# Performance work log

Measured on AMD Instinct MI355X. Metric: run time of the kernel, lower is better.

## Reference

```python
import jax, jax.numpy as jnp
import numpy as np

N, E = 25000, 400000
NF, EF, HNF, HEF = 32, 32, 128, 128
NOUT, EOUT = 32, 32
D_N, D_E = HNF + NF, HEF + EF  # concat dims fed to the GNN layer


def _glorot(key, shape):
    return jax.random.normal(key, shape, jnp.float32) / np.sqrt(shape[0])


def setup_inputs() -> dict:
    key = jax.random.key(0)
    ks = jax.random.split(key, 10)
    return {
        "nf": jax.random.normal(ks[0], (N, NF), jnp.float32),
        "ef": jax.random.normal(ks[1], (E, EF), jnp.float32),
        "src": jax.random.randint(ks[2], (E,), 0, N),
        "dst": jax.random.randint(ks[3], (E,), 0, N),
        # AttnMPNNLayer params: edge model, attention logit model, node model
        "W_edge": _glorot(ks[4], (2 * D_N + D_E, HEF)),
        "b_edge": jnp.zeros((HEF,), jnp.float32),
        "W_attn": _glorot(ks[5], (2 * D_N + D_E, 1)),
        "b_attn": jnp.zeros((1,), jnp.float32),
        "W_node": _glorot(ks[6], (D_N + HEF, HNF)),
        "b_node": jnp.zeros((HNF,), jnp.float32),
        # output heads (MLP with num_neurons=[] -> single Linear)
        "W_nout": _glorot(ks[7], (HNF, NOUT)),
        "b_nout": jnp.zeros((NOUT,), jnp.float32),
        "W_eout": _glorot(ks[8], (HEF, EOUT)),
        "b_eout": jnp.zeros((EOUT,), jnp.float32),
        "n_iters": 3,
    }


def _attn_mpnn_layer(hnf, hef, src, dst, W_edge, b_edge, W_attn, b_attn, W_node, b_node):
    """Attention message passing: gather endpoints, edge MLP + attn logit,
    edge-softmax over incoming edges (per dst node), scatter-aggregate, node MLP."""
    n = hnf.shape[0]
    e_in = jnp.concatenate([hnf[src], hnf[dst], hef], axis=-1)   # [E, 2*D_N + D_E]
    m = jax.nn.relu(e_in @ W_edge + b_edge)                      # [E, HEF] new edge feats
    logit = (e_in @ W_attn + b_attn)[:, 0]                       # [E]
    # numerically stable edge softmax grouped by destination node
    lmax = jax.ops.segment_max(logit, dst, num_segments=n)
    lmax = jnp.where(jnp.isfinite(lmax), lmax, 0.0)              # isolated nodes -> 0
    a = jnp.exp(logit - lmax[dst])
    denom = jax.ops.segment_sum(a, dst, num_segments=n)
    alpha = a / jnp.maximum(denom[dst], 1e-16)
    agg = jax.ops.segment_sum(alpha[:, None] * m, dst, num_segments=n)  # [N, HEF]
    un = jax.nn.relu(jnp.concatenate([hnf, agg], axis=-1) @ W_node + b_node)  # [N, HNF]
    return un, m


def reference(nf, ef, src, dst, W_edge, b_edge, W_attn, b_attn, W_node, b_node,
              W_nout, b_nout, W_eout, b_eout, n_iters):
    hnf = jnp.zeros((nf.shape[0], HNF), nf.dtype)
    hef = jnp.zeros((ef.shape[0], HEF), ef.dtype)
    for _ in range(n_iters):
        hnf = jnp.concatenate([hnf, nf], axis=-1)   # input re-injection
        hef = jnp.concatenate([hef, ef], axis=-1)
        hnf, hef = _attn_mpnn_layer(hnf, hef, src, dst,
                                    W_edge, b_edge, W_attn, b_attn, W_node, b_node)
    unf = hnf @ W_nout + b_nout
    uef = hef @ W_eout + b_eout
    return unf, uef
```

## Files before the change

kernel.cpp:

```cpp
#include <hip/hip_runtime.h>


#define GN 25000
#define GE 400000
#define NODE_BLKS 196
#define EDGE_BLKS 6250

typedef unsigned short u16;
typedef __attribute__((ext_vector_type(8))) short bf16x8;
typedef __attribute__((ext_vector_type(4))) float f32x4;

__device__ inline float b2f(u16 v) {
  union { unsigned int u; float f; } x; x.u = ((unsigned int)v) << 16; return x.f;
}
__device__ inline u16 f2b(float f) {
  union { float f; unsigned int u; } x; x.f = f;
  unsigned int u = x.u;
  u += 0x7fffu + ((u >> 16) & 1u);
  return (u16)(u >> 16);
}

__global__ void detect_dtype(const void* nf, int* flag) {
  if (blockIdx.x == 0 && threadIdx.x == 0) {
    const u16* p = (const u16*)nf;
    int cnt = 0;
    for (int i = 0; i < 512; i += 2) {
      int e = (p[i] >> 7) & 0xFF;
      if (e >= 0x70 && e <= 0x85) cnt++;
    }
    *flag = (cnt < 128) ? 1 : 0;
  }
}

__global__ void convert_kernel(const void* src, u16* dst, long n, const int* flag) {
  int f32 = *flag;
  long i = (long)blockIdx.x * blockDim.x + threadIdx.x;
  long stride = (long)gridDim.x * blockDim.x;
  for (; i < n; i += stride)
    dst[i] = f32 ? f2b(((const float*)src)[i]) : ((const u16*)src)[i];
}

__global__ void gather_ef(const void* ef, const int* eid, u16* efc, const int* flag) {
  int f32 = *flag;
  long idx = (long)blockIdx.x * blockDim.x + threadIdx.x;
  long ntot = (long)GE * 4;
  if (idx >= ntot) return;
  long j = idx >> 2;
  int g = (int)(idx & 3) * 8;
  long e = eid[j];
  uint4 out;
  if (f32) {
    const float* pf = (const float*)ef + e * 32 + g;
    float4 a = ((const float4*)pf)[0];
    float4 b = ((const float4*)pf)[1];
    unsigned int* ov = (unsigned int*)&out;
    ov[0] = (unsigned int)f2b(a.x) | ((unsigned int)f2b(a.y) << 16);
    ov[1] = (unsigned int)f2b(a.z) | ((unsigned int)f2b(a.w) << 16);
    ov[2] = (unsigned int)f2b(b.x) | ((unsigned int)f2b(b.y) << 16);
    ov[3] = (unsigned int)f2b(b.z) | ((unsigned int)f2b(b.w) << 16);
  } else {
    out = *(const uint4*)((const u16*)ef + e * 32 + g);
  }
  *(uint4*)(efc + j * 32 + g) = out;
}

__global__ void prep_weights(const void* We, const void* Wn, const void* Wa,
                             const void* Won, const void* Woe,
                             const void* be, const void* ba, const void* bn,
                             const void* bno, const void* beo,
                             u16* WeT, u16* WnpT, u16* WnuT, u16* WoN, u16* WoE,
                             u16* Wac, u16* bec, u16* bac, u16* bnc, u16* bnoc, u16* beoc,
                             const int* flag) {
  int f32 = *flag;
  auto ld = [&](const void* p, long i) -> u16 {
    return f32 ? f2b(((const float*)p)[i]) : ((const u16*)p)[i];
  };
  int tid = blockIdx.x * blockDim.x + threadIdx.x;
  int nt = gridDim.x * blockDim.x;
  for (int i = tid; i < 128 * 160; i += nt) { int n = i / 160, k = i % 160; WeT[i] = ld(We, (long)(320 + k) * 128 + n); }
  for (int i = tid; i < 256 * 160; i += nt) {
    int c = i / 160, k = i % 160;
    WnpT[i] = (c < 128) ? ld(We, (long)k * 128 + c) : ld(We, (long)(160 + k) * 128 + (c - 128));
  }
  for (int i = tid; i < 128 * 288; i += nt) { int c = i / 288, k = i % 288; WnuT[i] = ld(Wn, (long)k * 128 + c); }
  for (int i = tid; i < 32 * 128; i += nt) {
    int c = i / 128, k = i % 128;
    WoN[i] = ld(Won, (long)k * 32 + c);
    WoE[i] = ld(Woe, (long)k * 32 + c);
  }
  for (int i = tid; i < 480; i += nt) Wac[i] = ld(Wa, i);
  for (int i = tid; i < 128; i += nt) { bec[i] = ld(be, i); bnc[i] = ld(bn, i); }
  for (int i = tid; i < 32; i += nt) { bnoc[i] = ld(bno, i); beoc[i] = ld(beo, i); }
  if (tid == 0) bac[0] = ld(ba, 0);
}

__global__ void hist_kernel(const int* dst, int* counts, int n) {
  for (int e = blockIdx.x * blockDim.x + threadIdx.x; e < n; e += gridDim.x * blockDim.x)
    atomicAdd(&counts[dst[e]], 1);
}

__global__ __launch_bounds__(1024) void scan_kernel(int* cursor, int* rowptr, int n) {
  __shared__ int part[1024];
  int t = threadIdx.x;
  int per = (n + 1023) / 1024;
  int lo = t * per;
  int hi = lo + per; if (hi > n) hi = n;
  if (lo > n) lo = n;
  int s = 0;
  for (int i = lo; i < hi; ++i) s += cursor[i];
  part[t] = s;
  __syncthreads();
  for (int off = 1; off < 1024; off <<= 1) {
    int v = (t >= off) ? part[t - off] : 0;
    __syncthreads();
    part[t] += v;
    __syncthreads();
  }
  int run = (t > 0) ? part[t - 1] : 0;
  for (int i = lo; i < hi; ++i) {
    int c = cursor[i];
    cursor[i] = run;
    rowptr[i + 1] = run + c;
    run += c;
  }
  if (t == 0) rowptr[0] = 0;
}

__global__ void fill_kernel(const int* src, const int* dst, int* cursor, int* eid,
                            int* srcs, int* dsts, int n) {
  for (int e = blockIdx.x * blockDim.x + threadIdx.x; e < n; e += gridDim.x * blockDim.x) {
    int d = dst[e];
    int p = atomicAdd(&cursor[d], 1);
    eid[p] = e;
    srcs[p] = src[e];
    dsts[p] = d;
  }
}

__global__ __launch_bounds__(256)
void node_proj(const u16* HNF, const u16* nf, const u16* WnpT, const u16* W_attn,
               u16* Xs, u16* Xd, float* as_, float* ad_, int kc0, int nrows) {
  __shared__ union {
    struct { __align__(16) u16 A[128][40]; __align__(16) u16 B[128][40]; } st;
    u16 C[128][130];
  } sm;
  __shared__ float dotbuf[128][2];
  int sel = blockIdx.y, blk = blockIdx.x, tid = threadIdx.x;
  int lane = tid & 63, wv = tid >> 6, wr = wv & 1, wc = wv >> 1;
  const u16* BT = WnpT + sel * 128 * 160;
  u16* OUT = sel ? Xd : Xs;
  float* AOUT = sel ? ad_ : as_;
  const u16* wa = W_attn + sel * 160;
  f32x4 acc[4][4];
  f32x4 zf = {0.f, 0.f, 0.f, 0.f};
  for (int i = 0; i < 4; ++i) for (int j = 0; j < 4; ++j) acc[i][j] = zf;
  float dp = 0.f;
  int arow = tid >> 1, ahalf = (tid & 1) * 16;
  int r0 = blk * 128;
  int ra = r0 + arow;
  uint4 va0 = make_uint4(0, 0, 0, 0), va1 = make_uint4(0, 0, 0, 0), vb0, vb1;
  {
    if (ra < nrows) {
      const uint4* p = (kc0 < 4) ? (const uint4*)(HNF + (size_t)ra * 128 + kc0 * 32 + ahalf)
                                 : (const uint4*)(nf + (size_t)ra * 32 + ahalf);
      va0 = p[0]; va1 = p[1];
    }
    const uint4* pb = (const uint4*)(BT + arow * 160 + kc0 * 32 + ahalf);
    vb0 = pb[0]; vb1 = pb[1];
  }
  for (int kc = kc0; kc < 5; ++kc) {
    *(uint4*)&sm.st.A[arow][ahalf] = va0;
    *(uint4*)&sm.st.A[arow][ahalf + 8] = va1;
    *(uint4*)&sm.st.B[arow][ahalf] = vb0;
    *(uint4*)&sm.st.B[arow][ahalf + 8] = vb1;
    if (kc < 4) {
      int kn = kc + 1;
      va0 = make_uint4(0, 0, 0, 0); va1 = make_uint4(0, 0, 0, 0);
      if (ra < nrows) {
        const uint4* p = (kn < 4) ? (const uint4*)(HNF + (size_t)ra * 128 + kn * 32 + ahalf)
                                  : (const uint4*)(nf + (size_t)ra * 32 + ahalf);
        va0 = p[0]; va1 = p[1];
      }
      const uint4* pb = (const uint4*)(BT + arow * 160 + kn * 32 + ahalf);
      vb0 = pb[0]; vb1 = pb[1];
    }
    __syncthreads();
    {
      float s = 0.f;
      for (int j = 0; j < 16; ++j) s += b2f(sm.st.A[arow][ahalf + j]) * b2f(wa[kc * 32 + ahalf + j]);
      dp += s;
    }
    int q = lane >> 4, l16 = lane & 15;
    bf16x8 af[4], bfr[4];
    for (int i = 0; i < 4; ++i) af[i] = *(const bf16x8*)&sm.st.A[wr * 64 + i * 16 + l16][q * 8];
    for (int j = 0; j < 4; ++j) bfr[j] = *(const bf16x8*)&sm.st.B[wc * 64 + j * 16 + l16][q * 8];
    for (int i = 0; i < 4; ++i)
      for (int j = 0; j < 4; ++j)
        acc[i][j] = __builtin_amdgcn_mfma_f32_16x16x32_bf16(af[i], bfr[j], acc[i][j], 0, 0, 0);
    __syncthreads();
  }
  dotbuf[arow][tid & 1] = dp;
  {
    int q = lane >> 4, l16 = lane & 15;
    for (int i = 0; i < 4; ++i)
      for (int j = 0; j < 4; ++j) {
        int col = wc * 64 + j * 16 + l16;
        for (int rr = 0; rr < 4; ++rr) {
          int row = wr * 64 + i * 16 + q * 4 + rr;
          sm.C[row][col] = f2b(acc[i][j][rr]);
        }
      }
  }
  __syncthreads();
  if (tid < 128) {
    int r = r0 + tid;
    if (r < nrows) AOUT[r] = dotbuf[tid][0] + dotbuf[tid][1];
  }
  {
    int r = tid >> 1, h = (tid & 1) * 64;
    int rg = r0 + r;
    if (rg < nrows) {
      uint4* po = (uint4*)(OUT + (size_t)rg * 128 + h);
      for (int k = 0; k < 8; ++k) {
        unsigned int a0 = *(const unsigned int*)&sm.C[r][h + k * 8];
        unsigned int a1 = *(const unsigned int*)&sm.C[r][h + k * 8 + 2];
        unsigned int a2 = *(const unsigned int*)&sm.C[r][h + k * 8 + 4];
        unsigned int a3 = *(const unsigned int*)&sm.C[r][h + k * 8 + 6];
        po[k] = make_uint4(a0, a1, a2, a3);
      }
    }
  }
}

template <int KC0, int LAST>
__global__ __launch_bounds__(256, 4)
void edge_fused(u16* HEF, const u16* ef, const u16* WeT, const u16* W_attn,
                const u16* b_edge, const u16* b_attn, const int* srcs, const int* dsts,
                const u16* Xs, const u16* Xd, const float* as_, const float* ad_,
                float* logit, const u16* WoE, const u16* b_eout, const int* eid,
                float* out_ef) {
  __shared__ union {
    __align__(16) u16 A[2][64][40];
    float C[64][65];
  } sm;
  __shared__ float dotbuf[64];
  __shared__ __align__(16) u16 Mt[LAST ? 64 : 1][136];
  int blk = blockIdx.x, tid = threadIdx.x;
  int lane = tid & 63, wv = tid >> 6, wr = wv & 1, wc = wv >> 1;
  int q = lane >> 4, l16 = lane & 15;
  f32x4 acc[2][4];
  f32x4 zf = {0.f, 0.f, 0.f, 0.f};
  for (int i = 0; i < 2; ++i) for (int j = 0; j < 4; ++j) acc[i][j] = zf;
  float dp[2] = {0.f, 0.f};
  long e0 = (long)blk * 64;
  long ea = e0 + (tid >> 2);
  int qp = (tid & 3) * 8;
  const u16* wa = W_attn + 320;

  uint4 va = (KC0 < 4) ? *(const uint4*)(HEF + ea * 128 + KC0 * 32 + qp)
                       : *(const uint4*)(ef + ea * 32 + qp);
  bf16x8 bfp[2][4];
#pragma unroll
  for (int j = 0; j < 4; ++j)
    bfp[KC0 & 1][j] = *(const bf16x8*)(WeT + (size_t)(wc * 64 + j * 16 + l16) * 160 + KC0 * 32 + q * 8);

#pragma unroll
  for (int kc = KC0; kc < 5; ++kc) {
    int buf = kc & 1;
    *(uint4*)&sm.A[buf][tid >> 2][qp] = va;
    if (kc < 4) {
      va = (kc + 1 < 4) ? *(const uint4*)(HEF + ea * 128 + (kc + 1) * 32 + qp)
                        : *(const uint4*)(ef + ea * 32 + qp);
#pragma unroll
      for (int j = 0; j < 4; ++j)
        bfp[(kc + 1) & 1][j] = *(const bf16x8*)(WeT + (size_t)(wc * 64 + j * 16 + l16) * 160 + (kc + 1) * 32 + q * 8);
    }
    __syncthreads();
    bf16x8 af[2];
    for (int i = 0; i < 2; ++i) af[i] = *(const bf16x8*)&sm.A[buf][wr * 32 + i * 16 + l16][q * 8];
    if (wc == 0) {
      bf16x8 wv8 = *(const bf16x8*)&wa[kc * 32 + q * 8];
      float wf[8];
      for (int j = 0; j < 8; ++j) wf[j] = b2f((u16)wv8[j]);
      for (int i = 0; i < 2; ++i)
        for (int j = 0; j < 8; ++j) dp[i] += b2f((u16)af[i][j]) * wf[j];
    }
    for (int i = 0; i < 2; ++i)
      for (int j = 0; j < 4; ++j)
        acc[i][j] = __builtin_amdgcn_mfma_f32_16x16x32_bf16(af[i], bfp[buf][j], acc[i][j], 0, 0, 0);
  }
  if (wc == 0) {
    for (int i = 0; i < 2; ++i) {
      dp[i] += __shfl_xor(dp[i], 16);
      dp[i] += __shfl_xor(dp[i], 32);
    }
    if (q == 0)
      for (int i = 0; i < 2; ++i) dotbuf[wr * 32 + i * 16 + l16] = dp[i];
  }
  int r = tid >> 2, qh = tid & 3;
  long e = e0 + r;
  int s = srcs[e], d = dsts[e];
#pragma unroll
  for (int p = 0; p < 2; ++p) {
    int cb = p * 64 + qh * 16;
    const uint4* ps = (const uint4*)(Xs + (size_t)s * 128 + cb);
    const uint4* pd = (const uint4*)(Xd + (size_t)d * 128 + cb);
    uint4 gs0 = ps[0], gs1 = ps[1], gd0 = pd[0], gd1 = pd[1];
    __syncthreads();
    if (wc == p) {
      for (int i = 0; i < 2; ++i)
        for (int j = 0; j < 4; ++j) {
          int col = j * 16 + l16;
          float bb = b2f(b_edge[p * 64 + col]);
          for (int rr = 0; rr < 4; ++rr)
            sm.C[wr * 32 + i * 16 + q * 4 + rr][col] = acc[i][j][rr] + bb;
        }
    }
    __syncthreads();
    if (p == 0 && tid < 64) {
      long ee = e0 + tid;
      logit[ee] = dotbuf[tid] + as_[srcs[ee]] + ad_[dsts[ee]] + b2f(b_attn[0]);
    }
    unsigned int us[8], ud[8];
    *(uint4*)&us[0] = gs0; *(uint4*)&us[4] = gs1;
    *(uint4*)&ud[0] = gd0; *(uint4*)&ud[4] = gd1;
    unsigned int ov[8];
    for (int w = 0; w < 8; ++w) {
      float c0 = sm.C[r][qh * 16 + 2 * w];
      float c1 = sm.C[r][qh * 16 + 2 * w + 1];
      float v0 = c0 + b2f((u16)(us[w] & 0xffffu)) + b2f((u16)(ud[w] & 0xffffu));
      float v1 = c1 + b2f((u16)(us[w] >> 16)) + b2f((u16)(ud[w] >> 16));
      ov[w] = (unsigned int)f2b(fmaxf(v0, 0.f)) | ((unsigned int)f2b(fmaxf(v1, 0.f)) << 16);
    }
    if (LAST) {
      *(uint4*)&Mt[r][cb] = *(uint4*)&ov[0];
      *(uint4*)&Mt[r][cb + 8] = *(uint4*)&ov[4];
    }
    uint4* po = (uint4*)(HEF + e * 128 + cb);
    po[0] = *(uint4*)&ov[0];
    po[1] = *(uint4*)&ov[4];
  }
  if (LAST) {
    __syncthreads();
    f32x4 ha0 = zf, ha1 = zf;
#pragma unroll
    for (int kc2 = 0; kc2 < 4; ++kc2) {
      bf16x8 af2 = *(const bf16x8*)&Mt[wv * 16 + l16][kc2 * 32 + q * 8];
      bf16x8 b0 = *(const bf16x8*)(WoE + (size_t)l16 * 128 + kc2 * 32 + q * 8);
      bf16x8 b1 = *(const bf16x8*)(WoE + (size_t)(16 + l16) * 128 + kc2 * 32 + q * 8);
      ha0 = __builtin_amdgcn_mfma_f32_16x16x32_bf16(af2, b0, ha0, 0, 0, 0);
      ha1 = __builtin_amdgcn_mfma_f32_16x16x32_bf16(af2, b1, ha1, 0, 0, 0);
    }
    float bb0 = b2f(b_eout[l16]), bb1 = b2f(b_eout[16 + l16]);
    for (int rr = 0; rr < 4; ++rr) {
      long ee = e0 + wv * 16 + q * 4 + rr;
      long ro = eid[ee];
      out_ef[ro * 32 + l16] = ha0[rr] + bb0;
      out_ef[ro * 32 + 16 + l16] = ha1[rr] + bb1;
    }
  }
}

__global__ __launch_bounds__(256)
void aggregate(const int* rowptr, const float* logit, const u16* M, u16* AGG, int nrows) {
  int gw = (blockIdx.x * blockDim.x + threadIdx.x) >> 6;
  int lane = threadIdx.x & 63;
  if (gw >= nrows) return;
  int beg = rowptr[gw], end = rowptr[gw + 1];
  int sub = lane >> 3, cl = lane & 7;
  float mx = -1e30f;
  for (int j = beg + lane; j < end; j += 64) mx = fmaxf(mx, logit[j]);
  for (int off = 32; off > 0; off >>= 1) mx = fmaxf(mx, __shfl_xor(mx, off));
  float acc[16];
  for (int t = 0; t < 16; ++t) acc[t] = 0.f;
  float denom = 0.f;
  float wc = 0.f;
  uint4 m0c = make_uint4(0, 0, 0, 0), m1c = make_uint4(0, 0, 0, 0);
  {
    int j = beg + sub;
    if (j < end) {
      wc = __expf(logit[j] - mx);
      const uint4* mp = (const uint4*)(M + (size_t)j * 128 + cl * 16);
      m0c = mp[0]; m1c = mp[1];
    }
  }
  for (int j0 = beg; j0 < end; j0 += 8) {
    float wn = 0.f;
    uint4 m0n = make_uint4(0, 0, 0, 0), m1n = make_uint4(0, 0, 0, 0);
    int jn = j0 + 8 + sub;
    if (jn < end) {
      wn = __expf(logit[jn] - mx);
      const uint4* mp = (const uint4*)(M + (size_t)jn * 128 + cl * 16);
      m0n = mp[0]; m1n = mp[1];
    }
    denom += wc;
    const unsigned int* mw0 = (const unsigned int*)&m0c;
    const unsigned int* mw1 = (const unsigned int*)&m1c;
    for (int t = 0; t < 4; ++t) {
      acc[2 * t]     += wc * b2f((u16)(mw0[t] & 0xffffu));
      acc[2 * t + 1] += wc * b2f((u16)(mw0[t] >> 16));
      acc[8 + 2 * t]     += wc * b2f((u16)(mw1[t] & 0xffffu));
      acc[8 + 2 * t + 1] += wc * b2f((u16)(mw1[t] >> 16));
    }
    wc = wn; m0c = m0n; m1c = m1n;
  }
  denom += __shfl_xor(denom, 8);
  denom += __shfl_xor(denom, 16);
  denom += __shfl_xor(denom, 32);
  for (int t = 0; t < 16; ++t) {
    acc[t] += __shfl_xor(acc[t], 8);
    acc[t] += __shfl_xor(acc[t], 16);
    acc[t] += __shfl_xor(acc[t], 32);
  }
  float inv = 1.0f / fmaxf(denom, 1e-16f);
  if (sub == 0) {
    unsigned int ov[8];
    for (int t = 0; t < 8; ++t)
      ov[t] = (unsigned int)f2b(acc[2 * t] * inv) | ((unsigned int)f2b(acc[2 * t + 1] * inv) << 16);
    uint4* po = (uint4*)(AGG + (size_t)gw * 128 + cl * 16);
    po[0] = *(uint4*)&ov[0];
    po[1] = *(uint4*)&ov[4];
  }
}

template <int LAST>
__global__ __launch_bounds__(256)
void node_update(u16* HNF, const u16* nf, const u16* AGG, const u16* WnuT,
                 const u16* b_node, int kc0, int nrows,
                 const u16* WoN, const u16* b_nout, float* out_nf) {
  __shared__ union {
    struct { __align__(16) u16 A[128][40]; __align__(16) u16 B[128][40]; } st;
    u16 C[128][130];
  } sm;
  int blk = blockIdx.x, tid = threadIdx.x;
  int lane = tid & 63, wv = tid >> 6, wr = wv & 1, wc = wv >> 1;
  f32x4 acc[4][4];
  f32x4 zf = {0.f, 0.f, 0.f, 0.f};
  for (int i = 0; i < 4; ++i) for (int j = 0; j < 4; ++j) acc[i][j] = zf;
  int arow = tid >> 1, ahalf = (tid & 1) * 16;
  int r0 = blk * 128;
  int ra = r0 + arow;
  auto asrc = [&](int kc) -> const u16* {
    if (kc < 4) return HNF + (size_t)ra * 128 + kc * 32 + ahalf;
    if (kc == 4) return nf + (size_t)ra * 32 + ahalf;
    return AGG + (size_t)ra * 128 + (kc - 5) * 32 + ahalf;
  };
  uint4 va0 = make_uint4(0, 0, 0, 0), va1 = make_uint4(0, 0, 0, 0), vb0, vb1;
  {
    if (ra < nrows) {
      const uint4* p = (const uint4*)asrc(kc0);
      va0 = p[0]; va1 = p[1];
    }
    const uint4* pb = (const uint4*)(WnuT + arow * 288 + kc0 * 32 + ahalf);
    vb0 = pb[0]; vb1 = pb[1];
  }
  for (int kc = kc0; kc < 9; ++kc) {
    *(uint4*)&sm.st.A[arow][ahalf] = va0;
    *(uint4*)&sm.st.A[arow][ahalf + 8] = va1;
    *(uint4*)&sm.st.B[arow][ahalf] = vb0;
    *(uint4*)&sm.st.B[arow][ahalf + 8] = vb1;
    if (kc < 8) {
      int kn = kc + 1;
      va0 = make_uint4(0, 0, 0, 0); va1 = make_uint4(0, 0, 0, 0);
      if (ra < nrows) {
        const uint4* p = (const uint4*)asrc(kn);
        va0 = p[0]; va1 = p[1];
      }
      const uint4* pb = (const uint4*)(WnuT + arow * 288 + kn * 32 + ahalf);
      vb0 = pb[0]; vb1 = pb[1];
    }
    __syncthreads();
    int q = lane >> 4, l16 = lane & 15;
    bf16x8 af[4], bfr[4];
    for (int i = 0; i < 4; ++i) af[i] = *(const bf16x8*)&sm.st.A[wr * 64 + i * 16 + l16][q * 8];
    for (int j = 0; j < 4; ++j) bfr[j] = *(const bf16x8*)&sm.st.B[wc * 64 + j * 16 + l16][q * 8];
    for (int i = 0; i < 4; ++i)
      for (int j = 0; j < 4; ++j)
        acc[i][j] = __builtin_amdgcn_mfma_f32_16x16x32_bf16(af[i], bfr[j], acc[i][j], 0, 0, 0);
    __syncthreads();
  }
  int q = lane >> 4, l16 = lane & 15;
  for (int i = 0; i < 4; ++i)
    for (int j = 0; j < 4; ++j) {
      int col = wc * 64 + j * 16 + l16;
      float bb = b2f(b_node[col]);
      for (int rr = 0; rr < 4; ++rr) {
        int row = wr * 64 + i * 16 + q * 4 + rr;
        sm.C[row][col] = f2b(fmaxf(acc[i][j][rr] + bb, 0.f));
      }
    }
  __syncthreads();
  {
    int r = tid >> 1, h = (tid & 1) * 64;
    int rg = r0 + r;
    if (rg < nrows) {
      uint4* po = (uint4*)(HNF + (size_t)rg * 128 + h);
      for (int k = 0; k < 8; ++k) {
        unsigned int a0 = *(const unsigned int*)&sm.C[r][h + k * 8];
        unsigned int a1 = *(const unsigned int*)&sm.C[r][h + k * 8 + 2];
        unsigned int a2 = *(const unsigned int*)&sm.C[r][h + k * 8 + 4];
        unsigned int a3 = *(const unsigned int*)&sm.C[r][h + k * 8 + 6];
        po[k] = make_uint4(a0, a1, a2, a3);
      }
    }
  }
  if (LAST) {
    f32x4 ha[2][2];
    for (int i = 0; i < 2; ++i) for (int j = 0; j < 2; ++j) ha[i][j] = zf;
#pragma unroll
    for (int kc2 = 0; kc2 < 4; ++kc2) {
      bf16x8 af2[2], bf2[2];
      for (int i = 0; i < 2; ++i) {
        unsigned int* ap = (unsigned int*)&af2[i];
        int row = wv * 32 + i * 16 + l16;
        for (int w = 0; w < 4; ++w)
          ap[w] = *(const unsigned int*)&sm.C[row][kc2 * 32 + q * 8 + 2 * w];
      }
      for (int j = 0; j < 2; ++j)
        bf2[j] = *(const bf16x8*)(WoN + (size_t)(j * 16 + l16) * 128 + kc2 * 32 + q * 8);
      for (int i = 0; i < 2; ++i)
        for (int j = 0; j < 2; ++j)
          ha[i][j] = __builtin_amdgcn_mfma_f32_16x16x32_bf16(af2[i], bf2[j], ha[i][j], 0, 0, 0);
    }
    for (int i = 0; i < 2; ++i)
      for (int rr = 0; rr < 4; ++rr) {
        int rowg = r0 + wv * 32 + i * 16 + q * 4 + rr;
        if (rowg < nrows)
          for (int j = 0; j < 2; ++j)
            out_nf[(size_t)rowg * 32 + j * 16 + l16] = ha[i][j][rr] + b2f(b_nout[j * 16 + l16]);
      }
  }
}

extern "C" void kernel_launch(void* const* d_in, const int* in_sizes, int n_in,
                              void* d_out, int out_size, void* d_ws, size_t ws_size,
                              hipStream_t stream) {
  const size_t REQUIRED = 160000000;
  if (ws_size < REQUIRED) return;

  const void* nf_r = d_in[0];
  const void* ef_r = d_in[1];
  const int* src = (const int*)d_in[2];
  const int* dst = (const int*)d_in[3];

  char* ws = (char*)d_ws;
  auto alloc = [&](size_t bytes) {
    char* p = ws;
    ws += (bytes + 255) & ~(size_t)255;
    return p;
  };
  u16* HEF = (u16*)alloc((size_t)GE * 128 * 2);
  u16* HNF = (u16*)alloc((size_t)GN * 128 * 2);
  u16* Xs = (u16*)alloc((size_t)GN * 128 * 2);
  u16* Xd = (u16*)alloc((size_t)GN * 128 * 2);
  float* as_ = (float*)alloc((size_t)GN * 4);
  float* ad_ = (float*)alloc((size_t)GN * 4);
  float* logit = (float*)alloc((size_t)GE * 4);
  int* rowptr = (int*)alloc((size_t)(GN + 1) * 4);
  int* cursor = (int*)alloc((size_t)GN * 4);
  int* eid = (int*)alloc((size_t)GE * 4);
  int* srcs = (int*)alloc((size_t)GE * 4);
  int* dsts = (int*)alloc((size_t)GE * 4);
  u16* WeT = (u16*)alloc(128 * 160 * 2);
  u16* WnpT = (u16*)alloc(256 * 160 * 2);
  u16* WnuT = (u16*)alloc(128 * 288 * 2);
  u16* WoN = (u16*)alloc(32 * 128 * 2);
  u16* WoE = (u16*)alloc(32 * 128 * 2);
  u16* nfc = (u16*)alloc((size_t)GN * 32 * 2);
  u16* efc = (u16*)alloc((size_t)GE * 32 * 2);
  u16* bec = (u16*)alloc(128 * 2);
  u16* Wac = (u16*)alloc(480 * 2);
  u16* bac = (u16*)alloc(2);
  u16* bnc = (u16*)alloc(128 * 2);
  u16* bnoc = (u16*)alloc(32 * 2);
  u16* beoc = (u16*)alloc(32 * 2);
  int* dflag = (int*)alloc(4);
  u16* AGG = Xs;

  float* out_nf = (float*)d_out;
  float* out_ef = (float*)d_out + (size_t)GN * 32;

  detect_dtype<<<1, 64, 0, stream>>>(nf_r, dflag);
  hipMemsetAsync(cursor, 0, (size_t)GN * 4, stream);
  hist_kernel<<<1563, 256, 0, stream>>>(dst, cursor, GE);
  scan_kernel<<<1, 1024, 0, stream>>>(cursor, rowptr, GN);
  fill_kernel<<<1563, 256, 0, stream>>>(src, dst, cursor, eid, srcs, dsts, GE);

  convert_kernel<<<784, 256, 0, stream>>>(nf_r, nfc, (long)GN * 32, dflag);
  gather_ef<<<6250, 256, 0, stream>>>(ef_r, eid, efc, dflag);
  prep_weights<<<128, 256, 0, stream>>>(d_in[4], d_in[8], d_in[6], d_in[10], d_in[12],
                                        d_in[5], d_in[7], d_in[9], d_in[11], d_in[13],
                                        WeT, WnpT, WnuT, WoN, WoE,
                                        Wac, bec, bac, bnc, bnoc, beoc, dflag);

  for (int iter = 0; iter < 3; ++iter) {
    int kc0 = (iter == 0) ? 4 : 0;
    dim3 npgrid(NODE_BLKS, 2);
    node_proj<<<npgrid, 256, 0, stream>>>(HNF, nfc, WnpT, Wac, Xs, Xd, as_, ad_, kc0, GN);
    if (iter == 0)
      edge_fused<4, 0><<<EDGE_BLKS, 256, 0, stream>>>(HEF, efc, WeT, Wac, bec, bac, srcs, dsts,
                                                      Xs, Xd, as_, ad_, logit, WoE, beoc, eid, out_ef);
    else if (iter == 1)
      edge_fused<0, 0><<<EDGE_BLKS, 256, 0, stream>>>(HEF, efc, WeT, Wac, bec, bac, srcs, dsts,
                                                      Xs, Xd, as_, ad_, logit, WoE, beoc, eid, out_ef);
    else
      edge_fused<0, 1><<<EDGE_BLKS, 256, 0, stream>>>(HEF, efc, WeT, Wac, bec, bac, srcs, dsts,
                                                      Xs, Xd, as_, ad_, logit, WoE, beoc, eid, out_ef);
    aggregate<<<(GN + 3) / 4, 256, 0, stream>>>(rowptr, logit, HEF, AGG, GN);
    if (iter < 2)
      node_update<0><<<NODE_BLKS, 256, 0, stream>>>(HNF, nfc, AGG, WnuT, bnc, kc0, GN,
                                                    WoN, bnoc, out_nf);
    else
      node_update<1><<<NODE_BLKS, 256, 0, stream>>>(HNF, nfc, AGG, WnuT, bnc, kc0, GN,
                                                    WoN, bnoc, out_nf);
  }
}
```

Baseline: 593.5 us.

## Process multiple edge tiles per block, coalesce edge output, fold nf conversion

The edge kernel now loops over three 64-edge tiles per block (2084 blocks instead of 6250) and prefetches the next tile's first input chunk while the current tile finishes. In the last iteration, the edge output projection is staged through shared memory so each row is written with 16-byte vector stores instead of scattered scalar stores. The separate nf conversion kernel is folded into prep_weights to save a launch. The cost is fewer blocks for latency hiding and extra barriers per tile.

```diff
diff --git a/kernel.cpp b/kernel.cpp
--- a/kernel.cpp
+++ b/kernel.cpp
@@ -4,7 +4,9 @@
 #define GN 25000
 #define GE 400000
 #define NODE_BLKS 196
-#define EDGE_BLKS 6250
+#define EDGE_TILES 6250
+#define EDGE_TPB 3
+#define EDGE_BLKS 2084
 
 typedef unsigned short u16;
 typedef __attribute__((ext_vector_type(8))) short bf16x8;
@@ -30,14 +32,6 @@
     }
     *flag = (cnt < 128) ? 1 : 0;
   }
-}
-
-__global__ void convert_kernel(const void* src, u16* dst, long n, const int* flag) {
-  int f32 = *flag;
-  long i = (long)blockIdx.x * blockDim.x + threadIdx.x;
-  long stride = (long)gridDim.x * blockDim.x;
-  for (; i < n; i += stride)
-    dst[i] = f32 ? f2b(((const float*)src)[i]) : ((const u16*)src)[i];
 }
 
 __global__ void gather_ef(const void* ef, const int* eid, u16* efc, const int* flag) {
@@ -67,16 +61,17 @@
 __global__ void prep_weights(const void* We, const void* Wn, const void* Wa,
                              const void* Won, const void* Woe,
                              const void* be, const void* ba, const void* bn,
-                             const void* bno, const void* beo,
+                             const void* bno, const void* beo, const void* nf,
                              u16* WeT, u16* WnpT, u16* WnuT, u16* WoN, u16* WoE,
                              u16* Wac, u16* bec, u16* bac, u16* bnc, u16* bnoc, u16* beoc,
-                             const int* flag) {
+                             u16* nfc, const int* flag) {
   int f32 = *flag;
   auto ld = [&](const void* p, long i) -> u16 {
     return f32 ? f2b(((const float*)p)[i]) : ((const u16*)p)[i];
   };
   int tid = blockIdx.x * blockDim.x + threadIdx.x;
   int nt = gridDim.x * blockDim.x;
+  for (long i = tid; i < (long)GN * 32; i += nt) nfc[i] = ld(nf, i);
   for (int i = tid; i < 128 * 160; i += nt) { int n = i / 160, k = i % 160; WeT[i] = ld(We, (long)(320 + k) * 128 + n); }
   for (int i = tid; i < 256 * 160; i += nt) {
     int c = i / 160, k = i % 160;
@@ -245,118 +240,142 @@
   } sm;
   __shared__ float dotbuf[64];
   __shared__ __align__(16) u16 Mt[LAST ? 64 : 1][136];
-  int blk = blockIdx.x, tid = threadIdx.x;
+  int tid = threadIdx.x;
   int lane = tid & 63, wv = tid >> 6, wr = wv & 1, wc = wv >> 1;
   int q = lane >> 4, l16 = lane & 15;
-  f32x4 acc[2][4];
   f32x4 zf = {0.f, 0.f, 0.f, 0.f};
-  for (int i = 0; i < 2; ++i) for (int j = 0; j < 4; ++j) acc[i][j] = zf;
-  float dp[2] = {0.f, 0.f};
-  long e0 = (long)blk * 64;
-  long ea = e0 + (tid >> 2);
+  const u16* wa = W_attn + 320;
+  int t0 = blockIdx.x * EDGE_TPB;
+  int tend = t0 + EDGE_TPB; if (tend > EDGE_TILES) tend = EDGE_TILES;
+  int rofs = tid >> 2;
   int qp = (tid & 3) * 8;
-  const u16* wa = W_attn + 320;
-
-  uint4 va = (KC0 < 4) ? *(const uint4*)(HEF + ea * 128 + KC0 * 32 + qp)
-                       : *(const uint4*)(ef + ea * 32 + qp);
-  bf16x8 bfp[2][4];
+
+  uint4 va;
+  {
+    long ea = (long)t0 * 64 + rofs;
+    va = (KC0 < 4) ? *(const uint4*)(HEF + ea * 128 + KC0 * 32 + qp)
+                   : *(const uint4*)(ef + ea * 32 + qp);
+  }
+
+  for (int t = t0; t < tend; ++t) {
+    long e0 = (long)t * 64;
+    long ea = e0 + rofs;
+    f32x4 acc[2][4];
+    for (int i = 0; i < 2; ++i) for (int j = 0; j < 4; ++j) acc[i][j] = zf;
+    float dp[2] = {0.f, 0.f};
+    bf16x8 bfp[2][4];
 #pragma unroll
-  for (int j = 0; j < 4; ++j)
-    bfp[KC0 & 1][j] = *(const bf16x8*)(WeT + (size_t)(wc * 64 + j * 16 + l16) * 160 + KC0 * 32 + q * 8);
+    for (int j = 0; j < 4; ++j)
+      bfp[KC0 & 1][j] = *(const bf16x8*)(WeT + (size_t)(wc * 64 + j * 16 + l16) * 160 + KC0 * 32 + q * 8);
 
 #pragma unroll
-  for (int kc = KC0; kc < 5; ++kc) {
-    int buf = kc & 1;
-    *(uint4*)&sm.A[buf][tid >> 2][qp] = va;
-    if (kc < 4) {
-      va = (kc + 1 < 4) ? *(const uint4*)(HEF + ea * 128 + (kc + 1) * 32 + qp)
-                        : *(const uint4*)(ef + ea * 32 + qp);
+    for (int kc = KC0; kc < 5; ++kc) {
+      int buf = kc & 1;
+      *(uint4*)&sm.A[buf][rofs][qp] = va;
+      if (kc < 4) {
+        va = (kc + 1 < 4) ? *(const uint4*)(HEF + ea * 128 + (kc + 1) * 32 + qp)
+                          : *(const uint4*)(ef + ea * 32 + qp);
 #pragma unroll
-      for (int j = 0; j < 4; ++j)
-        bfp[(kc + 1) & 1][j] = *(const bf16x8*)(WeT + (size_t)(wc * 64 + j * 16 + l16) * 160 + (kc + 1) * 32 + q * 8);
+        for (int j = 0; j < 4; ++j)
+          bfp[(kc + 1) & 1][j] = *(const bf16x8*)(WeT + (size_t)(wc * 64 + j * 16 + l16) * 160 + (kc + 1) * 32 + q * 8);
+      } else if (t + 1 < tend) {
+        long ean = ea + 64;
+        va = (KC0 < 4) ? *(const uint4*)(HEF + ean * 128 + KC0 * 32 + qp)
+                       : *(const uint4*)(ef + ean * 32 + qp);
+      }
+      __syncthreads();
+      bf16x8 af[2];
+      for (int i = 0; i < 2; ++i) af[i] = *(const bf16x8*)&sm.A[buf][wr * 32 + i * 16 + l16][q * 8];
+      if (wc == 0) {
+        bf16x8 wv8 = *(const bf16x8*)&wa[kc * 32 + q * 8];
+        float wf[8];
+        for (int j = 0; j < 8; ++j) wf[j] = b2f((u16)wv8[j]);
+        for (int i = 0; i < 2; ++i)
+          for (int j = 0; j < 8; ++j) dp[i] += b2f((u16)af[i][j]) * wf[j];
+      }
+      for (int i = 0; i < 2; ++i)
+        for (int j = 0; j < 4; ++j)
+          acc[i][j] = __builtin_amdgcn_mfma_f32_16x16x32_bf16(af[i], bfp[buf][j], acc[i][j], 0, 0, 0);
+    }
+    if (wc == 0) {
+      for (int i = 0; i < 2; ++i) {
+        dp[i] += __shfl_xor(dp[i], 16);
+        dp[i] += __shfl_xor(dp[i], 32);
+      }
+      if (q == 0)
+        for (int i = 0; i < 2; ++i) dotbuf[wr * 32 + i * 16 + l16] = dp[i];
+    }
+    int r = tid >> 2, qh = tid & 3;
+    long e = e0 + r;
+    int s = srcs[e], d = dsts[e];
+#pragma unroll
+    for (int p = 0; p < 2; ++p) {
+      int cb = p * 64 + qh * 16;
+      const uint4* ps = (const uint4*)(Xs + (size_t)s * 128 + cb);
+      const uint4* pd = (const uint4*)(Xd + (size_t)d * 128 + cb);
+      uint4 gs0 = ps[0], gs1 = ps[1], gd0 = pd[0], gd1 = pd[1];
+      __syncthreads();
+      if (wc == p) {
+        for (int i = 0; i < 2; ++i)
+          for (int j = 0; j < 4; ++j) {
+            int col = j * 16 + l16;
+            float bb = b2f(b_edge[p * 64 + col]);
+            for (int rr = 0; rr < 4; ++rr)
+              sm.C[wr * 32 + i * 16 + q * 4 + rr][col] = acc[i][j][rr] + bb;
+          }
+      }
+      __syncthreads();
+      if (p == 0 && tid < 64) {
+        long ee = e0 + tid;
+        logit[ee] = dotbuf[tid] + as_[srcs[ee]] + ad_[dsts[ee]] + b2f(b_attn[0]);
+      }
+      unsigned int us[8], ud[8];
+      *(uint4*)&us[0] = gs0; *(uint4*)&us[4] = gs1;
+      *(uint4*)&ud[0] = gd0; *(uint4*)&ud[4] = gd1;
+      unsigned int ov[8];
+      for (int w = 0; w < 8; ++w) {
+        float c0 = sm.C[r][qh * 16 + 2 * w];
+        float c1 = sm.C[r][qh * 16 + 2 * w + 1];
+        float v0 = c0 + b2f((u16)(us[w] & 0xffffu)) + b2f((u16)(ud[w] & 0xffffu));
+        float v1 = c1 + b2f((u16)(us[w] >> 16)) + b2f((u16)(ud[w] >> 16));
+        ov[w] = (unsigned int)f2b(fmaxf(v0, 0.f)) | ((unsigned int)f2b(fmaxf(v1, 0.f)) << 16);
+      }
+      if constexpr (LAST) {
+        *(uint4*)&Mt[r][cb] = *(uint4*)&ov[0];
+        *(uint4*)&Mt[r][cb + 8] = *(uint4*)&ov[4];
+      }
+      uint4* po = (uint4*)(HEF + e * 128 + cb);
+      po[0] = *(uint4*)&ov[0];
+      po[1] = *(uint4*)&ov[4];
     }
     __syncthreads();
-    bf16x8 af[2];
-    for (int i = 0; i < 2; ++i) af[i] = *(const bf16x8*)&sm.A[buf][wr * 32 + i * 16 + l16][q * 8];
-    if (wc == 0) {
-      bf16x8 wv8 = *(const bf16x8*)&wa[kc * 32 + q * 8];
-      float wf[8];
-      for (int j = 0; j < 8; ++j) wf[j] = b2f((u16)wv8[j]);
-      for (int i = 0; i < 2; ++i)
-        for (int j = 0; j < 8; ++j) dp[i] += b2f((u16)af[i][j]) * wf[j];
-    }
-    for (int i = 0; i < 2; ++i)
-      for (int j = 0; j < 4; ++j)
-        acc[i][j] = __builtin_amdgcn_mfma_f32_16x16x32_bf16(af[i], bfp[buf][j], acc[i][j], 0, 0, 0);
-  }
-  if (wc == 0) {
-    for (int i = 0; i < 2; ++i) {
-      dp[i] += __shfl_xor(dp[i], 16);
-      dp[i] += __shfl_xor(dp[i], 32);
-    }
-    if (q == 0)
-      for (int i = 0; i < 2; ++i) dotbuf[wr * 32 + i * 16 + l16] = dp[i];
-  }
-  int r = tid >> 2, qh = tid & 3;
-  long e = e0 + r;
-  int s = srcs[e], d = dsts[e];
+    if constexpr (LAST) {
+      f32x4 ha0 = zf, ha1 = zf;
 #pragma unroll
-  for (int p = 0; p < 2; ++p) {
-    int cb = p * 64 + qh * 16;
-    const uint4* ps = (const uint4*)(Xs + (size_t)s * 128 + cb);
-    const uint4* pd = (const uint4*)(Xd + (size_t)d * 128 + cb);
-    uint4 gs0 = ps[0], gs1 = ps[1], gd0 = pd[0], gd1 = pd[1];
-    __syncthreads();
-    if (wc == p) {
-      for (int i = 0; i < 2; ++i)
-        for (int j = 0; j < 4; ++j) {
-          int col = j * 16 + l16;
-          float bb = b2f(b_edge[p * 64 + col]);
-          for (int rr = 0; rr < 4; ++rr)
-            sm.C[wr * 32 + i * 16 + q * 4 + rr][col] = acc[i][j][rr] + bb;
-        }
-    }
-    __syncthreads();
-    if (p == 0 && tid < 64) {
-      long ee = e0 + tid;
-      logit[ee] = dotbuf[tid] + as_[srcs[ee]] + ad_[dsts[ee]] + b2f(b_attn[0]);
-    }
-    unsigned int us[8], ud[8];
-    *(uint4*)&us[0] = gs0; *(uint4*)&us[4] = gs1;
-    *(uint4*)&ud[0] = gd0; *(uint4*)&ud[4] = gd1;
-    unsigned int ov[8];
-    for (int w = 0; w < 8; ++w) {
-      float c0 = sm.C[r][qh * 16 + 2 * w];
-      float c1 = sm.C[r][qh * 16 + 2 * w + 1];
-      float v0 = c0 + b2f((u16)(us[w] & 0xffffu)) + b2f((u16)(ud[w] & 0xffffu));
-      float v1 = c1 + b2f((u16)(us[w] >> 16)) + b2f((u16)(ud[w] >> 16));
-      ov[w] = (unsigned int)f2b(fmaxf(v0, 0.f)) | ((unsigned int)f2b(fmaxf(v1, 0.f)) << 16);
-    }
-    if (LAST) {
-      *(uint4*)&Mt[r][cb] = *(uint4*)&ov[0];
-      *(uint4*)&Mt[r][cb + 8] = *(uint4*)&ov[4];
-    }
-    uint4* po = (uint4*)(HEF + e * 128 + cb);
-    po[0] = *(uint4*)&ov[0];
-    po[1] = *(uint4*)&ov[4];
-  }
-  if (LAST) {
-    __syncthreads();
-    f32x4 ha0 = zf, ha1 = zf;
-#pragma unroll
-    for (int kc2 = 0; kc2 < 4; ++kc2) {
-      bf16x8 af2 = *(const bf16x8*)&Mt[wv * 16 + l16][kc2 * 32 + q * 8];
-      bf16x8 b0 = *(const bf16x8*)(WoE + (size_t)l16 * 128 + kc2 * 32 + q * 8);
-      bf16x8 b1 = *(const bf16x8*)(WoE + (size_t)(16 + l16) * 128 + kc2 * 32 + q * 8);
-      ha0 = __builtin_amdgcn_mfma_f32_16x16x32_bf16(af2, b0, ha0, 0, 0, 0);
-      ha1 = __builtin_amdgcn_mfma_f32_16x16x32_bf16(af2, b1, ha1, 0, 0, 0);
-    }
-    float bb0 = b2f(b_eout[l16]), bb1 = b2f(b_eout[16 + l16]);
-    for (int rr = 0; rr < 4; ++rr) {
-      long ee = e0 + wv * 16 + q * 4 + rr;
-      long ro = eid[ee];
-      out_ef[ro * 32 + l16] = ha0[rr] + bb0;
-      out_ef[ro * 32 + 16 + l16] = ha1[rr] + bb1;
+      for (int kc2 = 0; kc2 < 4; ++kc2) {
+        bf16x8 af2 = *(const bf16x8*)&Mt[wv * 16 + l16][kc2 * 32 + q * 8];
+        bf16x8 b0 = *(const bf16x8*)(WoE + (size_t)l16 * 128 + kc2 * 32 + q * 8);
+        bf16x8 b1 = *(const bf16x8*)(WoE + (size_t)(16 + l16) * 128 + kc2 * 32 + q * 8);
+        ha0 = __builtin_amdgcn_mfma_f32_16x16x32_bf16(af2, b0, ha0, 0, 0, 0);
+        ha1 = __builtin_amdgcn_mfma_f32_16x16x32_bf16(af2, b1, ha1, 0, 0, 0);
+      }
+      __syncthreads();
+      float* Mf = (float*)&Mt[0][0];
+      float bb0 = b2f(b_eout[l16]), bb1 = b2f(b_eout[16 + l16]);
+      for (int rr = 0; rr < 4; ++rr) {
+        int row = wv * 16 + q * 4 + rr;
+        Mf[row * 34 + l16] = ha0[rr] + bb0;
+        Mf[row * 34 + 16 + l16] = ha1[rr] + bb1;
+      }
+      __syncthreads();
+      {
+        int rr2 = tid >> 2, c0 = (tid & 3) * 8;
+        long ro = eid[e0 + rr2];
+        uint4 w0 = *(const uint4*)&Mf[rr2 * 34 + c0];
+        uint4 w1 = *(const uint4*)&Mf[rr2 * 34 + c0 + 4];
+        uint4* po = (uint4*)(out_ef + ro * 32 + c0);
+        po[0] = w0; po[1] = w1;
+      }
     }
   }
 }
@@ -504,7 +523,7 @@
       }
     }
   }
-  if (LAST) {
+  if constexpr (LAST) {
     f32x4 ha[2][2];
     for (int i = 0; i < 2; ++i) for (int j = 0; j < 2; ++j) ha[i][j] = zf;
 #pragma unroll
@@ -586,12 +605,11 @@
   scan_kernel<<<1, 1024, 0, stream>>>(cursor, rowptr, GN);
   fill_kernel<<<1563, 256, 0, stream>>>(src, dst, cursor, eid, srcs, dsts, GE);
 
-  convert_kernel<<<784, 256, 0, stream>>>(nf_r, nfc, (long)GN * 32, dflag);
   gather_ef<<<6250, 256, 0, stream>>>(ef_r, eid, efc, dflag);
   prep_weights<<<128, 256, 0, stream>>>(d_in[4], d_in[8], d_in[6], d_in[10], d_in[12],
-                                        d_in[5], d_in[7], d_in[9], d_in[11], d_in[13],
+                                        d_in[5], d_in[7], d_in[9], d_in[11], d_in[13], nf_r,
                                         WeT, WnpT, WnuT, WoN, WoE,
-                                        Wac, bec, bac, bnc, bnoc, beoc, dflag);
+                                        Wac, bec, bac, bnc, bnoc, beoc, nfc, dflag);
 
   for (int iter = 0; iter < 3; ++iter) {
     int kc0 = (iter == 0) ? 4 : 0;
```

Measured after the change: 880.3 us. +48.3%, slower.
